# Performance work log

Measured on AMD Instinct MI355X. Metric: run time of the kernel, lower is better.

## Reference

```python
import jax, jax.numpy as jnp
import numpy as np

H = 16       # num_attention_heads
KV = 4       # num_key_value_heads
HD = 128     # head_dim
BASE = 10000.0


def rotate_half(x):
    x1, x2 = jnp.split(x, 2, axis=-1)
    return jnp.concatenate((-x2, x1), axis=-1)


def rope_cos_sin(position_ids):
    # inv_freq: (HD/2,)
    inv_freq = 1.0 / (BASE ** (jnp.arange(0, HD, 2, dtype=jnp.float32) / HD))
    freqs = position_ids.astype(jnp.float32)[..., None] * inv_freq  # (B, S, HD/2)
    emb = jnp.concatenate((freqs, freqs), axis=-1)  # (B, S, HD)
    return jnp.cos(emb), jnp.sin(emb)


def setup_inputs() -> dict:
    key = jax.random.key(0)
    ks = jax.random.split(key, 5)
    B, S, D = 2, 2048, 2048
    sc = 1.0 / np.sqrt(D)
    return {
        "hidden_states": jax.random.normal(ks[0], (B, S, D), jnp.float32),
        "position_ids": jnp.broadcast_to(jnp.arange(S, dtype=jnp.int32), (B, S)),
        "wq": jax.random.normal(ks[1], (H * HD, D), jnp.float32) * sc,
        "wk": jax.random.normal(ks[2], (KV * HD, D), jnp.float32) * sc,
        "wv": jax.random.normal(ks[3], (KV * HD, D), jnp.float32) * sc,
        "wo": jax.random.normal(ks[4], (H * HD, H * HD), jnp.float32) * sc,
    }


def attention_forward(hidden_states, position_ids, wq, wk, wv, wo):
    B, S, D = hidden_states.shape
    n_rep = H // KV
    # projections -> (B, heads, S, HD)
    q = (hidden_states @ wq.T).reshape(B, S, H, HD).transpose(0, 2, 1, 3)
    k = (hidden_states @ wk.T).reshape(B, S, KV, HD).transpose(0, 2, 1, 3)
    v = (hidden_states @ wv.T).reshape(B, S, KV, HD).transpose(0, 2, 1, 3)
    # RoPE
    cos, sin = rope_cos_sin(position_ids)  # (B, S, HD)
    cos = cos[:, None]  # (B, 1, S, HD)
    sin = sin[:, None]
    q = q * cos + rotate_half(q) * sin
    k = k * cos + rotate_half(k) * sin
    # repeat kv heads for GQA: (B, KV, S, HD) -> (B, H, S, HD)
    k = jnp.repeat(k, n_rep, axis=1)
    v = jnp.repeat(v, n_rep, axis=1)
    scale = 1.0 / np.sqrt(HD)
    scores = jnp.einsum("bhqd,bhkd->bhqk", q, k) * scale
    attn = jax.nn.softmax(scores.astype(jnp.float32), axis=-1).astype(q.dtype)
    out = jnp.einsum("bhqk,bhkd->bhqd", attn, v)
    out = out.transpose(0, 2, 1, 3).reshape(B, S, H * HD)
    return out @ wo.T


def reference(hidden_states, position_ids, wq, wk, wv, wo):
    return attention_forward(hidden_states, position_ids, wq, wk, wv, wo)
```

## Files before the change

### kernel.cpp

```cpp
#include <hip/hip_runtime.h>
#include <hip/hip_bf16.h>
#include <math.h>


typedef __attribute__((ext_vector_type(4))) float f32x4;
typedef __attribute__((ext_vector_type(8))) short short8;
typedef __attribute__((ext_vector_type(4))) unsigned short u16x4;
typedef __attribute__((ext_vector_type(8))) unsigned short u16x8;

static __device__ __forceinline__ unsigned short f2bf(float x) {
    unsigned u = __builtin_bit_cast(unsigned, x);
    u += 0x7fffu + ((u >> 16) & 1u);
    return (unsigned short)(u >> 16);
}
static __device__ __forceinline__ float exp2_fast(float x) {
    float r;
    asm volatile("v_exp_f32 %0, %1" : "=v"(r) : "v"(x));
    return r;
}
static __device__ __forceinline__ unsigned cvt_pk_bf16(float a, float b) {
    unsigned r;
    asm("v_cvt_pk_bf16_f32 %0, %1, %2" : "=v"(r) : "v"(a), "v"(b));
    return r;
}
static __device__ __forceinline__ void gload16(const unsigned short* g, unsigned short* lds) {
    __builtin_amdgcn_global_load_lds((const __attribute__((address_space(1))) void*)g,
                                     (__attribute__((address_space(3))) void*)lds, 16, 0, 0);
}

__global__ __launch_bounds__(256) void k_prep(const float* __restrict__ hs,
                                              const float* __restrict__ wq,
                                              const float* __restrict__ wk,
                                              const float* __restrict__ wv,
                                              const float* __restrict__ wo,
                                              const int* __restrict__ pos_ids,
                                              unsigned short* __restrict__ hsb,
                                              unsigned short* __restrict__ wqkvb,
                                              unsigned short* __restrict__ wob,
                                              float2* __restrict__ tb) {
    long idx = (long)blockIdx.x * 256 + threadIdx.x;
    if (idx < 2097152) {
        f32x4 v = ((const f32x4*)hs)[idx];
        u16x4 o;
        o.x = f2bf(v.x); o.y = f2bf(v.y); o.z = f2bf(v.z); o.w = f2bf(v.w);
        ((u16x4*)hsb)[idx] = o;
    } else if (idx < 3670016) {
        long i = idx - 2097152;
        long flat = i * 4;
        int row = (int)(flat >> 11);
        int col = (int)(flat & 2047);
        const float* src;
        if (row < 2560) {
            int base = row & 2047;
            int hh = base >> 7, ii = base & 127;
            int d = (ii >> 1) + ((ii & 1) << 6);
            src = (row < 2048 ? wq : wk) + (size_t)(hh * 128 + d) * 2048;
        } else {
            src = wv + (size_t)(row - 2560) * 2048;
        }
        f32x4 v = *(const f32x4*)(src + col);
        u16x4 o;
        o.x = f2bf(v.x); o.y = f2bf(v.y); o.z = f2bf(v.z); o.w = f2bf(v.w);
        *(u16x4*)(wqkvb + flat) = o;
    } else if (idx < 4718592) {
        long i = idx - 3670016;
        f32x4 v = ((const f32x4*)wo)[i];
        u16x4 o;
        o.x = f2bf(v.x); o.y = f2bf(v.y); o.z = f2bf(v.z); o.w = f2bf(v.w);
        ((u16x4*)wob)[i] = o;
    } else {
        long j = idx - 4718592;
        int r = (int)(j >> 6);
        int i = (int)(j & 63);
        float pos = (float)pos_ids[r];
        float invf = exp2f((float)i * -0.20762050593046f);
        float arg  = pos * invf;
        float s, c;
        sincosf(arg, &s, &c);
        tb[(size_t)r * 64 + i] = make_float2(c, s);
    }
}

template <int EPI>
__global__ __launch_bounds__(256) void k_gemm(const unsigned short* __restrict__ A,
                                              const unsigned short* __restrict__ W,
                                              float* __restrict__ Cf,
                                              unsigned short* __restrict__ qkvt,
                                              unsigned short* __restrict__ vtb,
                                              const float2* __restrict__ tb,
                                              int M, int N, int K) {
    __shared__ unsigned short As[2][4096];
    __shared__ unsigned short Ws[2][4096];
    const int tid = threadIdx.x;
    const int lane = tid & 63;
    const int w = tid >> 6;
    const int q = lane & 15, g = lane >> 4;
    const int wr = w >> 1, wc = w & 1;

    const int nwg = gridDim.x * gridDim.y;
    const int id = blockIdx.y * gridDim.x + blockIdx.x;
    const int swz_id = (id & 7) * (nwg >> 3) + (id >> 3);
    const int bx = swz_id % gridDim.x;
    const int by = swz_id / gridDim.x;
    const long mbase = (long)by * 128;
    const long nbase = (long)bx * 128;

    const unsigned short* gA[2];
    const unsigned short* gW[2];
    #pragma unroll
    for (int j = 0; j < 2; ++j) {
        int r = j * 64 + (tid >> 2);
        int slot = (tid & 3) ^ ((r >> 1) & 3);
        gA[j] = A + (size_t)(mbase + r) * K + slot * 8;
        gW[j] = W + (size_t)(nbase + r) * K + slot * 8;
    }
    const int sa = (g ^ ((q >> 1) & 3)) * 8;

    f32x4 acc[4][4];
    #pragma unroll
    for (int m = 0; m < 4; ++m)
        #pragma unroll
        for (int n = 0; n < 4; ++n) acc[m][n] = (f32x4){0.f, 0.f, 0.f, 0.f};

    auto STAGE = [&](int buf) {
        #pragma unroll
        for (int j = 0; j < 2; ++j) {
            gload16(gA[j], &As[buf][j * 2048 + w * 512]);
            gload16(gW[j], &Ws[buf][j * 2048 + w * 512]);
            gA[j] += 32; gW[j] += 32;
        }
    };

    const int nk = K >> 5;
    STAGE(0);
    int cur = 0;
    for (int t = 0; t < nk; ++t) {
        if (t) __builtin_amdgcn_s_barrier();
        if (t + 1 < nk) {
            STAGE(cur ^ 1);
            asm volatile("s_waitcnt vmcnt(4)" ::: "memory");
        } else {
            asm volatile("s_waitcnt vmcnt(0)" ::: "memory");
        }
        __builtin_amdgcn_s_barrier();

        short8 af[4], bfr[4];
        #pragma unroll
        for (int m = 0; m < 4; ++m) af[m] = *(const short8*)&As[cur][(wr * 64 + m * 16 + q) * 32 + sa];
        #pragma unroll
        for (int n = 0; n < 4; ++n) bfr[n] = *(const short8*)&Ws[cur][(wc * 64 + n * 16 + q) * 32 + sa];
        #pragma unroll
        for (int m = 0; m < 4; ++m)
            #pragma unroll
            for (int n = 0; n < 4; ++n)
                acc[m][n] = __builtin_amdgcn_mfma_f32_16x16x32_bf16(af[m], bfr[n], acc[m][n], 0, 0, 0);
        cur ^= 1;
    }

    if (EPI == 0) {
        #pragma unroll
        for (int m = 0; m < 4; ++m)
            #pragma unroll
            for (int n = 0; n < 4; ++n)
                #pragma unroll
                for (int rr = 0; rr < 4; ++rr) {
                    long row = mbase + wr * 64 + m * 16 + 4 * g + rr;
                    long col = nbase + wc * 64 + n * 16 + q;
                    Cf[row * N + col] = acc[m][n][rr];
                }
    } else {
        const int tile = bx;
        if (tile >= 20) {
            const int kv = tile - 20;
            #pragma unroll
            for (int m = 0; m < 4; ++m)
                #pragma unroll
                for (int n = 0; n < 4; ++n) {
                    int c = wc * 64 + n * 16 + q;
                    long r0 = mbase + wr * 64 + m * 16 + 4 * g;
                    int b = (int)(r0 >> 11), s0 = (int)(r0 & 2047);
                    uint2 pk;
                    pk.x = cvt_pk_bf16(acc[m][n][0], acc[m][n][1]);
                    pk.y = cvt_pk_bf16(acc[m][n][2], acc[m][n][3]);
                    *(uint2*)(vtb + (size_t)((b * 4 + kv) * 128 + c) * 2048 + s0) = pk;
                }
        } else {
            const float scale = (tile < 16) ? 0.12751744f : 1.0f;
            const float sgn = (q & 1) ? 1.f : -1.f;
            #pragma unroll
            for (int m = 0; m < 4; ++m)
                #pragma unroll
                for (int rr = 0; rr < 4; ++rr) {
                    long row = mbase + wr * 64 + m * 16 + 4 * g + rr;
                    #pragma unroll
                    for (int n = 0; n < 4; ++n) {
                        int c = wc * 64 + n * 16 + q;
                        float x = acc[m][n][rr];
                        float p = __shfl_xor(x, 1);
                        float2 cs = tb[row * 64 + (c >> 1)];
                        float y = (x * cs.x + sgn * (p * cs.y)) * scale;
                        int dorig = (c >> 1) + ((c & 1) << 6);
                        long col = (tile < 16) ? (tile * 128 + dorig)
                                               : (2048 + (tile - 16) * 128 + dorig);
                        qkvt[row * 3072 + col] = f2bf(y);
                    }
                }
        }
    }
}

__global__ __launch_bounds__(256, 2) void k_flash(const unsigned short* __restrict__ qkv,
                                                  const unsigned short* __restrict__ vt,
                                                  unsigned short* __restrict__ aout) {
    __shared__ unsigned short Ks[2][8192];
    __shared__ unsigned short Vs[2][8192];
    __shared__ unsigned short Plds[4][1152];
    const int wg = blockIdx.x;
    const int kvg = wg & 7;
    const int inner = wg >> 3;
    const int h_in = inner & 3;
    const int qt = inner >> 2;
    const int b = kvg >> 2, kvh = kvg & 3;
    const int h = kvh * 4 + h_in;
    const int tid = threadIdx.x;
    const int w = tid >> 6, lane = tid & 63;
    const int q = lane & 15, g = lane >> 4;
    const int qrow = qt * 128 + w * 32;

    short8 qf[2][4];
    #pragma unroll
    for (int u = 0; u < 2; ++u) {
        const unsigned short* Qp = qkv + (size_t)(b * 2048 + qrow + u * 16 + q) * 3072 + h * 128 + g * 8;
        #pragma unroll
        for (int t = 0; t < 4; ++t) qf[u][t] = *(const short8*)(Qp + t * 32);
    }

    const unsigned short* Kbase = qkv + (size_t)(b * 2048) * 3072 + 2048 + kvh * 128;
    const unsigned short* Vbase = vt + (size_t)((b * 4 + kvh) * 128) * 2048;
    const unsigned short* gK[4];
    const unsigned short* gV[4];
    #pragma unroll
    for (int i = 0; i < 4; ++i) {
        int rowK = w * 16 + i * 4 + (lane >> 4);
        gK[i] = Kbase + (size_t)rowK * 3072 + (((lane & 15) ^ (rowK & 7)) << 3);
        int rowV = w * 32 + i * 8 + (lane >> 3);
        gV[i] = Vbase + (size_t)rowV * 2048 + (((lane & 7) ^ (rowV & 7)) << 3);
    }

    const int swz = (q & 7) << 3;
    int tcK[4];
    #pragma unroll
    for (int t = 0; t < 4; ++t) tcK[t] = (t * 32 + g * 8) ^ swz;

    unsigned short* Pw = Plds[w];

    float m_run[2] = {-INFINITY, -INFINITY};
    float l_run[2] = {0.f, 0.f};
    f32x4 o[2][8];
    #pragma unroll
    for (int u = 0; u < 2; ++u)
        #pragma unroll
        for (int nf = 0; nf < 8; ++nf) o[u][nf] = (f32x4){0.f, 0.f, 0.f, 0.f};

    auto STAGE = [&](int buf) {
        #pragma unroll
        for (int i = 0; i < 4; ++i) {
            gload16(gK[i], &Ks[buf][w * 2048 + i * 512]);
            gload16(gV[i], &Vs[buf][w * 2048 + i * 512]);
            gK[i] += 64 * 3072;
            gV[i] += 64;
        }
    };

    STAGE(0);
    int cur = 0;
    for (int t0 = 0; t0 < 32; ++t0) {
        if (t0 > 0) __builtin_amdgcn_s_barrier();
        if (t0 + 1 < 32) {
            STAGE(cur ^ 1);
            asm volatile("s_waitcnt vmcnt(8)" ::: "memory");
        } else {
            asm volatile("s_waitcnt vmcnt(0)" ::: "memory");
        }
        __builtin_amdgcn_s_barrier();

        const unsigned short* Kt = Ks[cur];
        const unsigned short* Vt = Vs[cur];

        f32x4 st[2][4];
        #pragma unroll
        for (int ks = 0; ks < 4; ++ks) {
            f32x4 a0 = (f32x4){0.f, 0.f, 0.f, 0.f};
            f32x4 a1 = (f32x4){0.f, 0.f, 0.f, 0.f};
            int rb = (ks * 16 + q) * 128;
            #pragma unroll
            for (int t = 0; t < 4; ++t) {
                short8 kf = *(const short8*)&Kt[rb + tcK[t]];
                a0 = __builtin_amdgcn_mfma_f32_16x16x32_bf16(kf, qf[0][t], a0, 0, 0, 0);
                a1 = __builtin_amdgcn_mfma_f32_16x16x32_bf16(kf, qf[1][t], a1, 0, 0, 0);
            }
            st[0][ks] = a0; st[1][ks] = a1;
        }

        short8 vf[8][2];
        #pragma unroll
        for (int nf = 0; nf < 8; ++nf) {
            int rb = (nf * 16 + q) * 64;
            #pragma unroll
            for (int t = 0; t < 2; ++t) vf[nf][t] = *(const short8*)&Vt[rb + tcK[t]];
        }

        #pragma unroll
        for (int u = 0; u < 2; ++u) {
            float mx = fmaxf(
                fmaxf(fmaxf(fmaxf(st[u][0][0], st[u][0][1]), fmaxf(st[u][0][2], st[u][0][3])),
                      fmaxf(fmaxf(st[u][1][0], st[u][1][1]), fmaxf(st[u][1][2], st[u][1][3]))),
                fmaxf(fmaxf(fmaxf(st[u][2][0], st[u][2][1]), fmaxf(st[u][2][2], st[u][2][3])),
                      fmaxf(fmaxf(st[u][3][0], st[u][3][1]), fmaxf(st[u][3][2], st[u][3][3]))));
            mx = fmaxf(mx, __shfl_xor(mx, 16));
            mx = fmaxf(mx, __shfl_xor(mx, 32));
            if (__any(mx - m_run[u] > 8.0f)) {
                float mn = fmaxf(m_run[u], mx);
                float sc = exp2_fast(m_run[u] - mn);
                l_run[u] *= sc;
                f32x4 sv;
                #pragma unroll
                for (int rr = 0; rr < 4; ++rr) sv[rr] = __shfl(sc, 4 * g + rr);
                #pragma unroll
                for (int nf = 0; nf < 8; ++nf) o[u][nf] *= sv;
                m_run[u] = mn;
            }
            f32x4 pe[4];
            #pragma unroll
            for (int ks = 0; ks < 4; ++ks)
                #pragma unroll
                for (int rr = 0; rr < 4; ++rr) pe[ks][rr] = exp2_fast(st[u][ks][rr] - m_run[u]);
            f32x4 ls4 = (pe[0] + pe[1]) + (pe[2] + pe[3]);
            float ls = (ls4[0] + ls4[1]) + (ls4[2] + ls4[3]);
            ls += __shfl_xor(ls, 16);
            ls += __shfl_xor(ls, 32);
            l_run[u] += ls;

            #pragma unroll
            for (int ks = 0; ks < 4; ++ks) {
                uint2 pk;
                pk.x = cvt_pk_bf16(pe[ks][0], pe[ks][1]);
                pk.y = cvt_pk_bf16(pe[ks][2], pe[ks][3]);
                *(uint2*)&Pw[q * 72 + ks * 16 + 4 * g] = pk;
            }
            asm volatile("s_waitcnt lgkmcnt(0)" ::: "memory");
            short8 pa0 = *(const short8*)&Pw[q * 72 + g * 8];
            short8 pa1 = *(const short8*)&Pw[q * 72 + 32 + g * 8];

            #pragma unroll
            for (int nf = 0; nf < 8; ++nf) {
                f32x4 a = o[u][nf];
                a = __builtin_amdgcn_mfma_f32_16x16x32_bf16(pa0, vf[nf][0], a, 0, 0, 0);
                a = __builtin_amdgcn_mfma_f32_16x16x32_bf16(pa1, vf[nf][1], a, 0, 0, 0);
                o[u][nf] = a;
            }
        }
        cur ^= 1;
    }

    #pragma unroll
    for (int u = 0; u < 2; ++u) {
        f32x4 li;
        #pragma unroll
        for (int rr = 0; rr < 4; ++rr) li[rr] = __shfl(l_run[u], 4 * g + rr);
        #pragma unroll
        for (int rr = 0; rr < 4; ++rr) li[rr] = 1.0f / li[rr];
        #pragma unroll
        for (int nf = 0; nf < 8; ++nf)
            #pragma unroll
            for (int rr = 0; rr < 4; ++rr) {
                size_t row = (size_t)(b * 2048 + qrow + u * 16 + 4 * g + rr);
                aout[row * 2048 + h * 128 + nf * 16 + q] = f2bf(o[u][nf][rr] * li[rr]);
            }
    }
}

extern "C" void kernel_launch(void* const* d_in, const int* in_sizes, int n_in,
                              void* d_out, int out_size, void* d_ws, size_t ws_size,
                              hipStream_t stream) {
    (void)in_sizes; (void)n_in; (void)out_size; (void)ws_size;
    const float* hs = (const float*)d_in[0];
    const int* pos  = (const int*)d_in[1];
    const float* wq = (const float*)d_in[2];
    const float* wk = (const float*)d_in[3];
    const float* wv = (const float*)d_in[4];
    const float* wo = (const float*)d_in[5];
    float* out = (float*)d_out;

    unsigned short* hsb   = (unsigned short*)d_ws;
    unsigned short* wqkvb = hsb + (size_t)4096 * 2048;
    unsigned short* wob   = wqkvb + (size_t)3072 * 2048;
    unsigned short* qkvt  = wob + (size_t)2048 * 2048;
    unsigned short* vtb   = qkvt + (size_t)4096 * 3072;
    float2* tb            = (float2*)(vtb + (size_t)8 * 128 * 2048);
    unsigned short* aoutb = (unsigned short*)(tb + (size_t)4096 * 64);

    k_prep<<<19456, 256, 0, stream>>>(hs, wq, wk, wv, wo, pos, hsb, wqkvb, wob, tb);
    k_gemm<1><<<dim3(24, 32), 256, 0, stream>>>(hsb, wqkvb, nullptr, qkvt, vtb, tb, 4096, 3072, 2048);
    k_flash<<<dim3(512), 256, 0, stream>>>(qkvt, vtb, aoutb);
    k_gemm<0><<<dim3(16, 32), 256, 0, stream>>>(aoutb, wob, out, nullptr, nullptr, nullptr, 4096, 2048, 2048);
}
```

Measured before the change: 220.1 us.

## Switch flash attention to 32x32x16 MFMA with register-resident P transpose

Rewrites the flash attention inner loop to use 32x32x16 bf16 MFMA tiles computing S^T so each lane owns one query row. The softmax max and sum reductions then need only one cross-lane shuffle, and the P matrix is rearranged into the B-operand layout with lane-xor-32 shuffles instead of a round trip through LDS. This removes the P shared buffer and its lgkmcnt wait and cuts the number of LDS fragment reads per tile. Output stores become packed 8-byte writes. The risk is higher register pressure from the 16-wide accumulators under a two-block occupancy bound.

```diff
diff --git a/kernel.cpp b/kernel.cpp
--- a/kernel.cpp
+++ b/kernel.cpp
@@ -4,7 +4,9 @@
 
 
 typedef __attribute__((ext_vector_type(4))) float f32x4;
+typedef __attribute__((ext_vector_type(16))) float f32x16;
 typedef __attribute__((ext_vector_type(8))) short short8;
+typedef __attribute__((ext_vector_type(4))) unsigned u32x4;
 typedef __attribute__((ext_vector_type(4))) unsigned short u16x4;
 typedef __attribute__((ext_vector_type(8))) unsigned short u16x8;
 
@@ -22,6 +24,10 @@
     unsigned r;
     asm("v_cvt_pk_bf16_f32 %0, %1, %2" : "=v"(r) : "v"(a), "v"(b));
     return r;
+}
+static __device__ __forceinline__ short8 pack4(unsigned a, unsigned b, unsigned c, unsigned d) {
+    u32x4 v; v.x = a; v.y = b; v.z = c; v.w = d;
+    return __builtin_bit_cast(short8, v);
 }
 static __device__ __forceinline__ void gload16(const unsigned short* g, unsigned short* lds) {
     __builtin_amdgcn_global_load_lds((const __attribute__((address_space(1))) void*)g,
@@ -214,7 +220,6 @@
                                                   unsigned short* __restrict__ aout) {
     __shared__ unsigned short Ks[2][8192];
     __shared__ unsigned short Vs[2][8192];
-    __shared__ unsigned short Plds[4][1152];
     const int wg = blockIdx.x;
     const int kvg = wg & 7;
     const int inner = wg >> 3;
@@ -224,15 +229,16 @@
     const int h = kvh * 4 + h_in;
     const int tid = threadIdx.x;
     const int w = tid >> 6, lane = tid & 63;
-    const int q = lane & 15, g = lane >> 4;
+    const int ql = lane & 31;
+    const int hi = lane >> 5;
+    const int q7 = ql & 7;
     const int qrow = qt * 128 + w * 32;
 
-    short8 qf[2][4];
-    #pragma unroll
-    for (int u = 0; u < 2; ++u) {
-        const unsigned short* Qp = qkv + (size_t)(b * 2048 + qrow + u * 16 + q) * 3072 + h * 128 + g * 8;
-        #pragma unroll
-        for (int t = 0; t < 4; ++t) qf[u][t] = *(const short8*)(Qp + t * 32);
+    short8 qf[8];
+    {
+        const unsigned short* Qp = qkv + (size_t)(b * 2048 + qrow + ql) * 3072 + h * 128 + hi * 8;
+        #pragma unroll
+        for (int s = 0; s < 8; ++s) qf[s] = *(const short8*)(Qp + s * 16);
     }
 
     const unsigned short* Kbase = qkv + (size_t)(b * 2048) * 3072 + 2048 + kvh * 128;
@@ -247,20 +253,12 @@
         gV[i] = Vbase + (size_t)rowV * 2048 + (((lane & 7) ^ (rowV & 7)) << 3);
     }
 
-    const int swz = (q & 7) << 3;
-    int tcK[4];
-    #pragma unroll
-    for (int t = 0; t < 4; ++t) tcK[t] = (t * 32 + g * 8) ^ swz;
-
-    unsigned short* Pw = Plds[w];
-
-    float m_run[2] = {-INFINITY, -INFINITY};
-    float l_run[2] = {0.f, 0.f};
-    f32x4 o[2][8];
-    #pragma unroll
-    for (int u = 0; u < 2; ++u)
-        #pragma unroll
-        for (int nf = 0; nf < 8; ++nf) o[u][nf] = (f32x4){0.f, 0.f, 0.f, 0.f};
+    float m_run = -INFINITY, l_run = 0.f;
+    f32x16 o[4];
+    #pragma unroll
+    for (int dt = 0; dt < 4; ++dt)
+        #pragma unroll
+        for (int j = 0; j < 16; ++j) o[dt][j] = 0.f;
 
     auto STAGE = [&](int buf) {
         #pragma unroll
@@ -287,97 +285,84 @@
         const unsigned short* Kt = Ks[cur];
         const unsigned short* Vt = Vs[cur];
 
-        f32x4 st[2][4];
-        #pragma unroll
-        for (int ks = 0; ks < 4; ++ks) {
-            f32x4 a0 = (f32x4){0.f, 0.f, 0.f, 0.f};
-            f32x4 a1 = (f32x4){0.f, 0.f, 0.f, 0.f};
-            int rb = (ks * 16 + q) * 128;
-            #pragma unroll
-            for (int t = 0; t < 4; ++t) {
-                short8 kf = *(const short8*)&Kt[rb + tcK[t]];
-                a0 = __builtin_amdgcn_mfma_f32_16x16x32_bf16(kf, qf[0][t], a0, 0, 0, 0);
-                a1 = __builtin_amdgcn_mfma_f32_16x16x32_bf16(kf, qf[1][t], a1, 0, 0, 0);
+        f32x16 st0, st1;
+        #pragma unroll
+        for (int j = 0; j < 16; ++j) { st0[j] = 0.f; st1[j] = 0.f; }
+        #pragma unroll
+        for (int s = 0; s < 8; ++s) {
+            int slot = ((2 * s + hi) ^ q7) * 8;
+            short8 kf0 = *(const short8*)&Kt[(ql) * 128 + slot];
+            short8 kf1 = *(const short8*)&Kt[(32 + ql) * 128 + slot];
+            st0 = __builtin_amdgcn_mfma_f32_32x32x16_bf16(kf0, qf[s], st0, 0, 0, 0);
+            st1 = __builtin_amdgcn_mfma_f32_32x32x16_bf16(kf1, qf[s], st1, 0, 0, 0);
+        }
+
+        float mx = -INFINITY;
+        #pragma unroll
+        for (int j = 0; j < 16; ++j) mx = fmaxf(mx, fmaxf(st0[j], st1[j]));
+        mx = fmaxf(mx, __shfl_xor(mx, 32));
+        if (__any(mx - m_run > 8.0f)) {
+            float mn = fmaxf(m_run, mx);
+            float sc = exp2_fast(m_run - mn);
+            l_run *= sc;
+            #pragma unroll
+            for (int dt = 0; dt < 4; ++dt)
+                #pragma unroll
+                for (int j = 0; j < 16; ++j) o[dt][j] *= sc;
+            m_run = mn;
+        }
+        float ls = 0.f;
+        #pragma unroll
+        for (int j = 0; j < 16; ++j) {
+            st0[j] = exp2_fast(st0[j] - m_run);
+            st1[j] = exp2_fast(st1[j] - m_run);
+            ls += st0[j] + st1[j];
+        }
+        ls += __shfl_xor(ls, 32);
+        l_run += ls;
+
+        short8 PB[4];
+        #pragma unroll
+        for (int tile = 0; tile < 2; ++tile) {
+            const f32x16& pe = tile ? st1 : st0;
+            unsigned W0 = cvt_pk_bf16(pe[0], pe[1]),   W1 = cvt_pk_bf16(pe[2], pe[3]);
+            unsigned W2 = cvt_pk_bf16(pe[4], pe[5]),   W3 = cvt_pk_bf16(pe[6], pe[7]);
+            unsigned W4 = cvt_pk_bf16(pe[8], pe[9]),   W5 = cvt_pk_bf16(pe[10], pe[11]);
+            unsigned W6 = cvt_pk_bf16(pe[12], pe[13]), W7 = cvt_pk_bf16(pe[14], pe[15]);
+            unsigned S1 = (unsigned)__shfl_xor((int)(hi ? W0 : W2), 32);
+            unsigned S2 = (unsigned)__shfl_xor((int)(hi ? W1 : W3), 32);
+            unsigned S3 = (unsigned)__shfl_xor((int)(hi ? W4 : W6), 32);
+            unsigned S4 = (unsigned)__shfl_xor((int)(hi ? W5 : W7), 32);
+            PB[tile * 2 + 0] = hi ? pack4(S1, S2, W2, W3) : pack4(W0, W1, S1, S2);
+            PB[tile * 2 + 1] = hi ? pack4(S3, S4, W6, W7) : pack4(W4, W5, S3, S4);
+        }
+
+        #pragma unroll
+        for (int dt = 0; dt < 4; ++dt) {
+            int vrb = (dt * 32 + ql) * 64;
+            f32x16 a = o[dt];
+            #pragma unroll
+            for (int ks = 0; ks < 4; ++ks) {
+                int slot = ((2 * ks + hi) ^ q7) * 8;
+                short8 vf = *(const short8*)&Vt[vrb + slot];
+                a = __builtin_amdgcn_mfma_f32_32x32x16_bf16(vf, PB[ks], a, 0, 0, 0);
             }
-            st[0][ks] = a0; st[1][ks] = a1;
-        }
-
-        short8 vf[8][2];
-        #pragma unroll
-        for (int nf = 0; nf < 8; ++nf) {
-            int rb = (nf * 16 + q) * 64;
-            #pragma unroll
-            for (int t = 0; t < 2; ++t) vf[nf][t] = *(const short8*)&Vt[rb + tcK[t]];
-        }
-
-        #pragma unroll
-        for (int u = 0; u < 2; ++u) {
-            float mx = fmaxf(
-                fmaxf(fmaxf(fmaxf(st[u][0][0], st[u][0][1]), fmaxf(st[u][0][2], st[u][0][3])),
-                      fmaxf(fmaxf(st[u][1][0], st[u][1][1]), fmaxf(st[u][1][2], st[u][1][3]))),
-                fmaxf(fmaxf(fmaxf(st[u][2][0], st[u][2][1]), fmaxf(st[u][2][2], st[u][2][3])),
-                      fmaxf(fmaxf(st[u][3][0], st[u][3][1]), fmaxf(st[u][3][2], st[u][3][3]))));
-            mx = fmaxf(mx, __shfl_xor(mx, 16));
-            mx = fmaxf(mx, __shfl_xor(mx, 32));
-            if (__any(mx - m_run[u] > 8.0f)) {
-                float mn = fmaxf(m_run[u], mx);
-                float sc = exp2_fast(m_run[u] - mn);
-                l_run[u] *= sc;
-                f32x4 sv;
-                #pragma unroll
-                for (int rr = 0; rr < 4; ++rr) sv[rr] = __shfl(sc, 4 * g + rr);
-                #pragma unroll
-                for (int nf = 0; nf < 8; ++nf) o[u][nf] *= sv;
-                m_run[u] = mn;
-            }
-            f32x4 pe[4];
-            #pragma unroll
-            for (int ks = 0; ks < 4; ++ks)
-                #pragma unroll
-                for (int rr = 0; rr < 4; ++rr) pe[ks][rr] = exp2_fast(st[u][ks][rr] - m_run[u]);
-            f32x4 ls4 = (pe[0] + pe[1]) + (pe[2] + pe[3]);
-            float ls = (ls4[0] + ls4[1]) + (ls4[2] + ls4[3]);
-            ls += __shfl_xor(ls, 16);
-            ls += __shfl_xor(ls, 32);
-            l_run[u] += ls;
-
-            #pragma unroll
-            for (int ks = 0; ks < 4; ++ks) {
-                uint2 pk;
-                pk.x = cvt_pk_bf16(pe[ks][0], pe[ks][1]);
-                pk.y = cvt_pk_bf16(pe[ks][2], pe[ks][3]);
-                *(uint2*)&Pw[q * 72 + ks * 16 + 4 * g] = pk;
-            }
-            asm volatile("s_waitcnt lgkmcnt(0)" ::: "memory");
-            short8 pa0 = *(const short8*)&Pw[q * 72 + g * 8];
-            short8 pa1 = *(const short8*)&Pw[q * 72 + 32 + g * 8];
-
-            #pragma unroll
-            for (int nf = 0; nf < 8; ++nf) {
-                f32x4 a = o[u][nf];
-                a = __builtin_amdgcn_mfma_f32_16x16x32_bf16(pa0, vf[nf][0], a, 0, 0, 0);
-                a = __builtin_amdgcn_mfma_f32_16x16x32_bf16(pa1, vf[nf][1], a, 0, 0, 0);
-                o[u][nf] = a;
-            }
+            o[dt] = a;
         }
         cur ^= 1;
     }
 
-    #pragma unroll
-    for (int u = 0; u < 2; ++u) {
-        f32x4 li;
-        #pragma unroll
-        for (int rr = 0; rr < 4; ++rr) li[rr] = __shfl(l_run[u], 4 * g + rr);
-        #pragma unroll
-        for (int rr = 0; rr < 4; ++rr) li[rr] = 1.0f / li[rr];
-        #pragma unroll
-        for (int nf = 0; nf < 8; ++nf)
-            #pragma unroll
-            for (int rr = 0; rr < 4; ++rr) {
-                size_t row = (size_t)(b * 2048 + qrow + u * 16 + 4 * g + rr);
-                aout[row * 2048 + h * 128 + nf * 16 + q] = f2bf(o[u][nf][rr] * li[rr]);
-            }
-    }
+    float li = 1.0f / l_run;
+    unsigned short* op = aout + (size_t)(b * 2048 + qrow + ql) * 2048 + h * 128;
+    #pragma unroll
+    for (int dt = 0; dt < 4; ++dt)
+        #pragma unroll
+        for (int rq = 0; rq < 4; ++rq) {
+            uint2 pk;
+            pk.x = cvt_pk_bf16(o[dt][rq * 4 + 0] * li, o[dt][rq * 4 + 1] * li);
+            pk.y = cvt_pk_bf16(o[dt][rq * 4 + 2] * li, o[dt][rq * 4 + 3] * li);
+            *(uint2*)(op + dt * 32 + rq * 8 + hi * 4) = pk;
+        }
 }
 
 extern "C" void kernel_launch(void* const* d_in, const int* in_sizes, int n_in,
```

After: 223.6 us. Within noise of the previous version (+1.6%).

## Enlarge flash-attention tiles to 256 query rows and 128-key blocks with 8 waves

Applied to the files above, without the earlier changes.

The flash kernel now runs 512-thread workgroups with 8 waves covering 256 query rows. Each iteration stages a 128-key K/V block, so there are 16 iterations instead of 32. V fragments are loaded from LDS just in time inside the PV loop and shared across both query sub-tiles, which is meant to halve barrier and softmax-rescale overhead per key and improve K/V reuse. The cost is twice the LDS footprint (about 137KB per block), fewer workgroups (256), and higher register pressure from st[2][8], all of which may lower occupancy.

```diff
diff --git a/kernel.cpp b/kernel.cpp
--- a/kernel.cpp
+++ b/kernel.cpp
@@ -209,12 +209,12 @@
     }
 }
 
-__global__ __launch_bounds__(256, 2) void k_flash(const unsigned short* __restrict__ qkv,
+__global__ __launch_bounds__(512, 2) void k_flash(const unsigned short* __restrict__ qkv,
                                                   const unsigned short* __restrict__ vt,
                                                   unsigned short* __restrict__ aout) {
-    __shared__ unsigned short Ks[2][8192];
-    __shared__ unsigned short Vs[2][8192];
-    __shared__ unsigned short Plds[4][1152];
+    __shared__ unsigned short Ks[2][16384];
+    __shared__ unsigned short Vs[2][16384];
+    __shared__ unsigned short Plds[8][1152];
     const int wg = blockIdx.x;
     const int kvg = wg & 7;
     const int inner = wg >> 3;
@@ -225,7 +225,7 @@
     const int tid = threadIdx.x;
     const int w = tid >> 6, lane = tid & 63;
     const int q = lane & 15, g = lane >> 4;
-    const int qrow = qt * 128 + w * 32;
+    const int qrow = qt * 256 + w * 32;
 
     short8 qf[2][4];
     #pragma unroll
@@ -241,16 +241,16 @@
     const unsigned short* gV[4];
     #pragma unroll
     for (int i = 0; i < 4; ++i) {
-        int rowK = w * 16 + i * 4 + (lane >> 4);
-        gK[i] = Kbase + (size_t)rowK * 3072 + (((lane & 15) ^ (rowK & 7)) << 3);
-        int rowV = w * 32 + i * 8 + (lane >> 3);
-        gV[i] = Vbase + (size_t)rowV * 2048 + (((lane & 7) ^ (rowV & 7)) << 3);
-    }
-
-    const int swz = (q & 7) << 3;
-    int tcK[4];
-    #pragma unroll
-    for (int t = 0; t < 4; ++t) tcK[t] = (t * 32 + g * 8) ^ swz;
+        int rK = i * 32 + (tid >> 4);
+        int sl = ((tid & 15) ^ (rK & 7)) << 3;
+        gK[i] = Kbase + (size_t)rK * 3072 + sl;
+        gV[i] = Vbase + (size_t)rK * 2048 + sl;
+    }
+
+    const int q7 = q & 7;
+    int tc[4];
+    #pragma unroll
+    for (int t = 0; t < 4; ++t) tc[t] = (((t * 4 + g) ^ q7) << 3);
 
     unsigned short* Pw = Plds[w];
 
@@ -265,18 +265,18 @@
     auto STAGE = [&](int buf) {
         #pragma unroll
         for (int i = 0; i < 4; ++i) {
-            gload16(gK[i], &Ks[buf][w * 2048 + i * 512]);
-            gload16(gV[i], &Vs[buf][w * 2048 + i * 512]);
-            gK[i] += 64 * 3072;
-            gV[i] += 64;
+            gload16(gK[i], &Ks[buf][i * 4096 + w * 512]);
+            gload16(gV[i], &Vs[buf][i * 4096 + w * 512]);
+            gK[i] += 128 * 3072;
+            gV[i] += 128;
         }
     };
 
     STAGE(0);
     int cur = 0;
-    for (int t0 = 0; t0 < 32; ++t0) {
+    for (int t0 = 0; t0 < 16; ++t0) {
         if (t0 > 0) __builtin_amdgcn_s_barrier();
-        if (t0 + 1 < 32) {
+        if (t0 + 1 < 16) {
             STAGE(cur ^ 1);
             asm volatile("s_waitcnt vmcnt(8)" ::: "memory");
         } else {
@@ -287,36 +287,30 @@
         const unsigned short* Kt = Ks[cur];
         const unsigned short* Vt = Vs[cur];
 
-        f32x4 st[2][4];
-        #pragma unroll
-        for (int ks = 0; ks < 4; ++ks) {
+        f32x4 st[2][8];
+        #pragma unroll
+        for (int ks = 0; ks < 8; ++ks) {
             f32x4 a0 = (f32x4){0.f, 0.f, 0.f, 0.f};
             f32x4 a1 = (f32x4){0.f, 0.f, 0.f, 0.f};
             int rb = (ks * 16 + q) * 128;
             #pragma unroll
             for (int t = 0; t < 4; ++t) {
-                short8 kf = *(const short8*)&Kt[rb + tcK[t]];
+                short8 kf = *(const short8*)&Kt[rb + tc[t]];
                 a0 = __builtin_amdgcn_mfma_f32_16x16x32_bf16(kf, qf[0][t], a0, 0, 0, 0);
                 a1 = __builtin_amdgcn_mfma_f32_16x16x32_bf16(kf, qf[1][t], a1, 0, 0, 0);
             }
             st[0][ks] = a0; st[1][ks] = a1;
         }
 
-        short8 vf[8][2];
-        #pragma unroll
-        for (int nf = 0; nf < 8; ++nf) {
-            int rb = (nf * 16 + q) * 64;
-            #pragma unroll
-            for (int t = 0; t < 2; ++t) vf[nf][t] = *(const short8*)&Vt[rb + tcK[t]];
-        }
-
         #pragma unroll
         for (int u = 0; u < 2; ++u) {
-            float mx = fmaxf(
-                fmaxf(fmaxf(fmaxf(st[u][0][0], st[u][0][1]), fmaxf(st[u][0][2], st[u][0][3])),
-                      fmaxf(fmaxf(st[u][1][0], st[u][1][1]), fmaxf(st[u][1][2], st[u][1][3]))),
-                fmaxf(fmaxf(fmaxf(st[u][2][0], st[u][2][1]), fmaxf(st[u][2][2], st[u][2][3])),
-                      fmaxf(fmaxf(st[u][3][0], st[u][3][1]), fmaxf(st[u][3][2], st[u][3][3]))));
+            f32x4 m4 = st[u][0];
+            #pragma unroll
+            for (int ks = 1; ks < 8; ++ks) {
+                #pragma unroll
+                for (int rr = 0; rr < 4; ++rr) m4[rr] = fmaxf(m4[rr], st[u][ks][rr]);
+            }
+            float mx = fmaxf(fmaxf(m4[0], m4[1]), fmaxf(m4[2], m4[3]));
             mx = fmaxf(mx, __shfl_xor(mx, 16));
             mx = fmaxf(mx, __shfl_xor(mx, 32));
             if (__any(mx - m_run[u] > 8.0f)) {
@@ -330,34 +324,47 @@
                 for (int nf = 0; nf < 8; ++nf) o[u][nf] *= sv;
                 m_run[u] = mn;
             }
-            f32x4 pe[4];
-            #pragma unroll
-            for (int ks = 0; ks < 4; ++ks)
-                #pragma unroll
-                for (int rr = 0; rr < 4; ++rr) pe[ks][rr] = exp2_fast(st[u][ks][rr] - m_run[u]);
-            f32x4 ls4 = (pe[0] + pe[1]) + (pe[2] + pe[3]);
-            float ls = (ls4[0] + ls4[1]) + (ls4[2] + ls4[3]);
+            f32x4 acc4 = (f32x4){0.f, 0.f, 0.f, 0.f};
+            #pragma unroll
+            for (int ks = 0; ks < 8; ++ks) {
+                #pragma unroll
+                for (int rr = 0; rr < 4; ++rr) st[u][ks][rr] = exp2_fast(st[u][ks][rr] - m_run[u]);
+                acc4 += st[u][ks];
+            }
+            float ls = (acc4[0] + acc4[1]) + (acc4[2] + acc4[3]);
             ls += __shfl_xor(ls, 16);
             ls += __shfl_xor(ls, 32);
             l_run[u] += ls;
-
-            #pragma unroll
-            for (int ks = 0; ks < 4; ++ks) {
-                uint2 pk;
-                pk.x = cvt_pk_bf16(pe[ks][0], pe[ks][1]);
-                pk.y = cvt_pk_bf16(pe[ks][2], pe[ks][3]);
-                *(uint2*)&Pw[q * 72 + ks * 16 + 4 * g] = pk;
-            }
-            asm volatile("s_waitcnt lgkmcnt(0)" ::: "memory");
-            short8 pa0 = *(const short8*)&Pw[q * 72 + g * 8];
-            short8 pa1 = *(const short8*)&Pw[q * 72 + 32 + g * 8];
-
+        }
+
+        #pragma unroll
+        for (int s = 0; s < 2; ++s) {
+            short8 pa[2][2];
+            #pragma unroll
+            for (int u = 0; u < 2; ++u) {
+                #pragma unroll
+                for (int kk = 0; kk < 4; ++kk) {
+                    f32x4 pv = st[u][s * 4 + kk];
+                    uint2 pk;
+                    pk.x = cvt_pk_bf16(pv[0], pv[1]);
+                    pk.y = cvt_pk_bf16(pv[2], pv[3]);
+                    *(uint2*)&Pw[q * 72 + kk * 16 + 4 * g] = pk;
+                }
+                asm volatile("s_waitcnt lgkmcnt(0)" ::: "memory");
+                pa[u][0] = *(const short8*)&Pw[q * 72 + g * 8];
+                pa[u][1] = *(const short8*)&Pw[q * 72 + 32 + g * 8];
+            }
             #pragma unroll
             for (int nf = 0; nf < 8; ++nf) {
-                f32x4 a = o[u][nf];
-                a = __builtin_amdgcn_mfma_f32_16x16x32_bf16(pa0, vf[nf][0], a, 0, 0, 0);
-                a = __builtin_amdgcn_mfma_f32_16x16x32_bf16(pa1, vf[nf][1], a, 0, 0, 0);
-                o[u][nf] = a;
+                int rb = (nf * 16 + q) * 128;
+                short8 v0 = *(const short8*)&Vt[rb + tc[2 * s]];
+                short8 v1 = *(const short8*)&Vt[rb + tc[2 * s + 1]];
+                f32x4 a0 = o[0][nf], a1 = o[1][nf];
+                a0 = __builtin_amdgcn_mfma_f32_16x16x32_bf16(pa[0][0], v0, a0, 0, 0, 0);
+                a0 = __builtin_amdgcn_mfma_f32_16x16x32_bf16(pa[0][1], v1, a0, 0, 0, 0);
+                a1 = __builtin_amdgcn_mfma_f32_16x16x32_bf16(pa[1][0], v0, a1, 0, 0, 0);
+                a1 = __builtin_amdgcn_mfma_f32_16x16x32_bf16(pa[1][1], v1, a1, 0, 0, 0);
+                o[0][nf] = a0; o[1][nf] = a1;
             }
         }
         cur ^= 1;
@@ -402,6 +409,6 @@
 
     k_prep<<<19456, 256, 0, stream>>>(hs, wq, wk, wv, wo, pos, hsb, wqkvb, wob, tb);
     k_gemm<1><<<dim3(24, 32), 256, 0, stream>>>(hsb, wqkvb, nullptr, qkvt, vtb, tb, 4096, 3072, 2048);
-    k_flash<<<dim3(512), 256, 0, stream>>>(qkvt, vtb, aoutb);
+    k_flash<<<dim3(256), 512, 0, stream>>>(qkvt, vtb, aoutb);
     k_gemm<0><<<dim3(16, 32), 256, 0, stream>>>(aoutb, wob, out, nullptr, nullptr, nullptr, 4096, 2048, 2048);
 }
```

Measured after the change: 215.4 us, median of 2. 1.02x faster.
